# Optimization experiments

Measured on AMD Instinct MI355X. Metric: run time of the kernel, lower is better.

Reference implementation:

```python
import jax, jax.numpy as jnp
from jax import lax
import numpy as np

NBITS = 3  # PartialSumLSQ bit width


def binarize(x):
    # straight-through sign (Binarize in BNN code modifies .data -> identity STE)
    return x + lax.stop_gradient(jnp.sign(x) - x)


def lsq(y, alpha):
    # LSQ quantizer for partial sums: q = round(clamp(y/a, Qn, Qp)) * a, STE round,
    # gradient-scaled step size (forward value unaffected by g).
    Qn, Qp = -(2 ** (NBITS - 1)), 2 ** (NBITS - 1) - 1
    g = 1.0 / np.sqrt(y.size * Qp)
    a = alpha * g + lax.stop_gradient(alpha - alpha * g)
    yc = jnp.clip(y / a, Qn, Qp)
    yq = yc + lax.stop_gradient(jnp.round(yc) - yc)
    return yq * a


def split_slices(xp, cgroups):
    # xp: [B, 128*cgroups, H+2, W+2]; reproduces split_tensor_128/256/512 ordering:
    # channel group outermost, then col offset j, then row offset i.
    H, W = xp.shape[2] - 2, xp.shape[3] - 2
    sl = [xp[:, g * 128:(g + 1) * 128, i:i + H, j:j + W]
          for g in range(cgroups) for j in range(3) for i in range(3)]
    return jnp.stack(sl)  # [S, B, 128, H, W]


def psum_stage(x, w, b, alpha, cgroups):
    # emulated 3x3 binary conv: pad, split into S shifted 128-ch slices, per-slice
    # binarized 1x1 conv + bias, LSQ-quantize each partial sum, accumulate.
    xp = jnp.pad(binarize(x), ((0, 0), (0, 0), (1, 1), (1, 1)))
    xs = split_slices(xp, cgroups)                      # [S,B,128,H,W]
    y = jnp.einsum('sbchw,soc->sbohw', xs, binarize(w)) + b[:, None, :, None, None]
    return jax.vmap(lsq)(y, alpha).sum(0)               # [B,Cout,H,W]


def maxpool2(x):
    return lax.reduce_window(x, -jnp.inf, lax.max, (1, 1, 2, 2), (1, 1, 2, 2), 'VALID')


def bn(x, g, b):
    # eval-mode BatchNorm with running_mean=0, running_var=1 -> affine
    s = (1, -1) + (1,) * (x.ndim - 2)
    return x * g.reshape(s) + b.reshape(s)


def htanh(x):
    return jnp.clip(x, -1.0, 1.0)


def _forward(x, conv1_w, conv1_b, s2_w, s2_b, s2_a, s3_w, s3_b, s3_a,
             s4_w, s4_b, s4_a, s5_w, s5_b, s5_a, s6_w, s6_b, s6_a,
             bn1_g, bn1_b, bn2_g, bn2_b, bn3_g, bn3_b, bn4_g, bn4_b,
             bn5_g, bn5_b, bn6_g, bn6_b, fc1_w, fc1_b, fc2_w, fc2_b,
             fc3_w, fc3_b, fbn1_g, fbn1_b, fbn2_g, fbn2_b, fbn3_g, fbn3_b):
    # conv1: 3->128 3x3 pad1; input has 3 channels -> not binarized, weight binarized
    h = lax.conv_general_dilated(x, binarize(conv1_w), (1, 1), ((1, 1), (1, 1)),
                                 dimension_numbers=('NCHW', 'OIHW', 'NCHW'))
    h = h + conv1_b[None, :, None, None]
    h = htanh(bn(h, bn1_g, bn1_b))
    h = psum_stage(h, s2_w, s2_b, s2_a, 1)   # 128->128, 9 slices, 32x32
    h = maxpool2(h)                          # 16x16
    h = htanh(bn(h, bn2_g, bn2_b))
    h = psum_stage(h, s3_w, s3_b, s3_a, 1)   # 128->256, 9 slices
    h = htanh(bn(h, bn3_g, bn3_b))
    h = psum_stage(h, s4_w, s4_b, s4_a, 2)   # 256->256, 18 slices
    h = maxpool2(h)                          # 8x8
    h = htanh(bn(h, bn4_g, bn4_b))
    h = psum_stage(h, s5_w, s5_b, s5_a, 2)   # 256->512, 18 slices
    h = htanh(bn(h, bn5_g, bn5_b))
    h = psum_stage(h, s6_w, s6_b, s6_a, 4)   # 512->512, 36 slices
    h = maxpool2(h)                          # 4x4
    h = htanh(bn(h, bn6_g, bn6_b))
    # binarized classifier: 512*4*4 -> 1024 -> 1024 -> num_classes
    f = binarize(h.reshape(h.shape[0], -1))
    f = f @ binarize(fc1_w).T + fc1_b
    f = htanh(f * fbn1_g + fbn1_b)
    f = binarize(f) @ binarize(fc2_w).T + fc2_b
    f = htanh(f * fbn2_g + fbn2_b)
    f = binarize(f) @ binarize(fc3_w).T + fc3_b
    return f * fbn3_g + fbn3_b


def setup_inputs() -> dict:
    key = jax.random.key(0)
    ks = iter(jax.random.split(key, 80))
    def rn(shape, scale=1.0):
        return jax.random.normal(next(ks), shape, jnp.float32) * scale
    d = {}
    d['x'] = rn((64, 3, 32, 32))
    d['conv1_w'] = rn((128, 3, 3, 3), 0.1)
    d['conv1_b'] = rn((128,), 0.01)
    stages = {'s2': (9, 128), 's3': (9, 256), 's4': (18, 256),
              's5': (18, 512), 's6': (36, 512)}
    for name, (S, co) in stages.items():
        d[name + '_w'] = rn((S, co, 128), 0.1)
        d[name + '_b'] = rn((S, co), 0.01)
        d[name + '_a'] = jax.random.uniform(next(ks), (S,), jnp.float32, 0.05, 0.15)
    for i, c in zip(range(1, 7), [128, 128, 256, 256, 512, 512]):
        d[f'bn{i}_g'] = jnp.ones((c,), jnp.float32) + rn((c,), 0.01)
        d[f'bn{i}_b'] = rn((c,), 0.01)
    d['fc1_w'] = rn((1024, 512 * 16), 0.02); d['fc1_b'] = rn((1024,), 0.01)
    d['fc2_w'] = rn((1024, 1024), 0.02);     d['fc2_b'] = rn((1024,), 0.01)
    d['fc3_w'] = rn((10, 1024), 0.02);       d['fc3_b'] = rn((10,), 0.01)
    for i, c in zip(range(1, 4), [1024, 1024, 10]):
        d[f'fbn{i}_g'] = jnp.ones((c,), jnp.float32) + rn((c,), 0.01)
        d[f'fbn{i}_b'] = rn((c,), 0.01)
    return d


def reference(x, conv1_w, conv1_b, s2_w, s2_b, s2_a, s3_w, s3_b, s3_a,
              s4_w, s4_b, s4_a, s5_w, s5_b, s5_a, s6_w, s6_b, s6_a,
              bn1_g, bn1_b, bn2_g, bn2_b, bn3_g, bn3_b, bn4_g, bn4_b,
              bn5_g, bn5_b, bn6_g, bn6_b, fc1_w, fc1_b, fc2_w, fc2_b,
              fc3_w, fc3_b, fbn1_g, fbn1_b, fbn2_g, fbn2_b, fbn3_g, fbn3_b):
    return _forward(x, conv1_w, conv1_b, s2_w, s2_b, s2_a, s3_w, s3_b, s3_a,
                    s4_w, s4_b, s4_a, s5_w, s5_b, s5_a, s6_w, s6_b, s6_a,
                    bn1_g, bn1_b, bn2_g, bn2_b, bn3_g, bn3_b, bn4_g, bn4_b,
                    bn5_g, bn5_b, bn6_g, bn6_b, fc1_w, fc1_b, fc2_w, fc2_b,
                    fc3_w, fc3_b, fbn1_g, fbn1_b, fbn2_g, fbn2_b, fbn3_g, fbn3_b)
```

## Files before the change

kernel.cpp:

```cpp
#include <hip/hip_runtime.h>
#include <hip/hip_bf16.h>
#include <math.h>

typedef unsigned long long u64;

struct PrepArgs {
    const float* w[7];
    u64* out[7];
    int cnt[7];
    int mode[7];
    const float* fc1w;
    u64* fc1T;
    const float* alpha[5];
    const float* bias[5];
    int loff[5];
    int lCout[5];
    double gq[5];
    u64* wlut;
    int R1, R2, R3;
};

__global__ __launch_bounds__(256)
void k_prep(PrepArgs A) {
    int gid = blockIdx.x * 256 + threadIdx.x;
    int lane = threadIdx.x & 63;
    if (gid < A.R1) {
        int wid = gid >> 6;
        int seg = 0, base = 0, pre = 0;
#pragma unroll
        for (int t = 0; t < 7; ++t) {
            if (wid >= pre) { seg = t; base = pre; }
            pre += A.cnt[t];
        }
        int li = wid - base;
        const float* p = A.w[seg] + ((size_t)li << 6);
        u64 m = __ballot(p[lane] > 0.f);
        if (lane == 0) {
            int mode = A.mode[seg];
            size_t idx = (mode == 1) ? ((size_t)(li >> 1) * 4 + (li & 1))
                       : (mode == 2) ? ((size_t)(li & 15) * 1024 + (li >> 4))
                       : (size_t)li;
            A.out[seg][idx] = m;
        }
    } else if (gid < A.R2) {
        int wid = (gid - A.R1) >> 6;
        int row = wid >> 3, gk = wid & 7;
        int g = gk >> 1, k = gk & 1;
        int c = g * 128 + k * 64 + lane;
        const float* p = A.fc1w + (size_t)row * 8192 + (size_t)c * 16;
        float arr[16];
#pragma unroll
        for (int q = 0; q < 4; ++q) {
            float4 f = ((const float4*)p)[q];
            arr[4 * q + 0] = f.x; arr[4 * q + 1] = f.y;
            arr[4 * q + 2] = f.z; arr[4 * q + 3] = f.w;
        }
#pragma unroll
        for (int h = 0; h < 4; ++h)
#pragma unroll
        for (int xq = 0; xq < 4; ++xq) {
            u64 m = __ballot(arr[h * 4 + xq] > 0.f);
            if (lane == 0) {
                int wd = g * 32 + h * 8 + xq * 2 + k;
                A.fc1T[(size_t)wd * 1024 + row] = m;
            }
        }
    } else if (gid < A.R3) {
        int idx = gid - A.R2;
        int seg = 0;
#pragma unroll
        for (int t = 1; t < 5; ++t) if (idx >= A.loff[t]) seg = t;
        int li = idx - A.loff[seg];
        int s = li / A.lCout[seg];
        double al = (double)A.alpha[seg][s];
        double tg = al * A.gq[seg];
        double a  = tg + (al - tg);
        double b  = (double)A.bias[seg][li];
        double q0 = rint(fmin(fmax(b / a, -4.0), 3.0));
        double qp = rint(fmin(fmax((2.0 + b) / a, -4.0), 3.0));
        double qn = rint(fmin(fmax((-2.0 + b) / a, -4.0), 3.0));
        double cz = q0 * a;
        double dp = qp * a - cz, dn = qn * a - cz;
        A.wlut[(size_t)idx * 4 + 2] = __double_as_longlong(0.5 * (dp + dn));
        A.wlut[(size_t)idx * 4 + 3] = __double_as_longlong(0.5 * (dp - dn));
    }
}

struct PvArgs {
    const float* alpha[5];
    const float* bias[5];
    int rowoff[5];
    int czoff[5];
    int S[5];
    int Cout[5];
    double gq[5];
    int total;
};

__global__ void k_pv(PvArgs A, const u64* __restrict__ wlut,
                     double* __restrict__ czv, double* __restrict__ pvt) {
    int idx = blockIdx.x * blockDim.x + threadIdx.x;
    if (idx >= A.total) return;
    int seg = 0;
#pragma unroll
    for (int t = 1; t < 5; ++t) if (idx >= A.czoff[t]) seg = t;
    int o = idx - A.czoff[seg];
    int Cout = A.Cout[seg];
    double CZ = 0.0;
    double pv[8] = {0, 0, 0, 0, 0, 0, 0, 0};
    for (int s = 0; s < A.S[seg]; ++s) {
        double al = (double)A.alpha[seg][s];
        double tg = al * A.gq[seg];
        double a  = tg + (al - tg);
        double b  = (double)A.bias[seg][s * Cout + o];
        double q0 = rint(fmin(fmax(b / a, -4.0), 3.0));
        CZ += q0 * a;
        size_t so = (size_t)(A.rowoff[seg] + s * Cout + o);
        const u64* wl = wlut + so * 4;
        u64 w0 = wl[0], w1 = wl[1];
        double mid  = __longlong_as_double(wl[2]);
        double half = __longlong_as_double(wl[3]);
        int e0 = 64 - (__popcll(w0) + __popcll(w1));
        int sg = min(max(e0, -1), 1);
        double sd = (double)sg;
        double pvv = fma(sd, fma(mid, sd, half), 0.0);
        int i3 = s % 3, j3 = (s / 3) % 3;
        if (i3 == 0) { pv[0] += pvv; if (j3 == 0) pv[4] += pvv; if (j3 == 2) pv[6] += pvv; }
        if (i3 == 2) { pv[1] += pvv; if (j3 == 0) pv[5] += pvv; if (j3 == 2) pv[7] += pvv; }
        if (j3 == 0) pv[2] += pvv;
        if (j3 == 2) pv[3] += pvv;
    }
    czv[idx] = CZ;
#pragma unroll
    for (int k = 0; k < 8; ++k) pvt[(size_t)idx * 8 + k] = pv[k];
}

__global__ __launch_bounds__(128)
void k_conv1(const float* __restrict__ x, const float* __restrict__ w,
             const float* __restrict__ cb, const float* __restrict__ g1,
             const float* __restrict__ b1, u64* __restrict__ apack) {
    __shared__ double xs[3][3][34];
    int h = blockIdx.x & 31;
    int b = blockIdx.x >> 5;
    int tid = threadIdx.x;
    for (int idx = tid; idx < 306; idx += 128) {
        int dyy = idx / 102;
        int rem = idx - dyy * 102;
        int ci = rem / 34;
        int col = rem - ci * 34;
        int y = h + dyy - 1, xx = col - 1;
        double v = 0.0;
        if ((unsigned)y < 32u && (unsigned)xx < 32u)
            v = (double)x[((b * 3 + ci) * 32 + y) * 32 + xx];
        xs[dyy][ci][col] = v;
    }
    __syncthreads();
    int o = tid;
    double sg[3][3][3];
#pragma unroll
    for (int ci = 0; ci < 3; ++ci)
#pragma unroll
    for (int ky = 0; ky < 3; ++ky)
#pragma unroll
    for (int kx = 0; kx < 3; ++kx) {
        float wv = w[o * 27 + (ci * 3 + ky) * 3 + kx];
        sg[kx][ci][ky] = wv > 0.f ? 1.0 : (wv < 0.f ? -1.0 : 0.0);
    }
    double cbv = (double)cb[o], g1v = (double)g1[o], b1v = (double)b1[o];
    double A0 = 0.0, A1 = 0.0, A2 = 0.0;
    for (int pc = 0; pc < 34; ++pc) {
        double v[3][3];
#pragma unroll
        for (int ky = 0; ky < 3; ++ky)
#pragma unroll
        for (int ci = 0; ci < 3; ++ci)
            v[ky][ci] = xs[ky][ci][pc];
        A2 = 0.0;
#pragma unroll
        for (int ci = 0; ci < 3; ++ci)
#pragma unroll
        for (int ky = 0; ky < 3; ++ky) {
            A0 += v[ky][ci] * sg[2][ci][ky];
            A1 += v[ky][ci] * sg[1][ci][ky];
            A2 += v[ky][ci] * sg[0][ci][ky];
        }
        if (pc >= 2) {
            int wc = pc - 2;
            double t = (A0 + cbv) * g1v + b1v;
            u64 m = __ballot(t > 0.0);
            if ((tid & 63) == 0)
                apack[((size_t)(b * 1024 + h * 32 + wc)) * 2 + (tid >> 6)] = m;
        }
        A0 = A1; A1 = A2;
    }
}

template <int POOL, int G, int H, int W, int Cout, int RCH, int NCH>
__global__ __launch_bounds__(64 * RCH * NCH)
void k_stage(const u64* __restrict__ apack, const u64* __restrict__ wlut,
             const double* __restrict__ czv, const double* __restrict__ pvt,
             const float* __restrict__ gam, const float* __restrict__ bet,
             u64* __restrict__ opack) {
    constexpr int CW = W / NCH;
    constexpr int Ho = H / POOL, Wo = W / POOL;
    constexpr int NOC = Cout / 64;
    constexpr int NRB = H / RCH;
    constexpr int NT = 64 * RCH * NCH;
    constexpr int NR = RCH + 2;
    constexpr int NCOL = W + 2;
    __shared__ alignas(16) u64 sact[G][NR][NCOL][2];
    constexpr int PLP = (POOL == 2) ? (RCH / 2) : 1;
    constexpr int PLN = (POOL == 2) ? NCH : 1;
    constexpr int PLC = (POOL == 2) ? (CW / 2) : 1;
    __shared__ double pl[PLP][PLN][PLC][64];

    int bi = blockIdx.x;
    int och = bi % NOC; bi /= NOC;
    int rb = bi % NRB;
    int b = bi / NRB;
    int tid = threadIdx.x;
    int ol = tid & 63;
    int rr = tid >> 6;
    int rc = rr / NCH;
    int nc = rr - rc * NCH;
    int o = och * 64 + ol;
    int yr = rb * RCH + rc;
    int c0 = nc * CW;

    for (int t = tid; t < G * NR * NCOL; t += NT) {
        int g = t / (NR * NCOL);
        int r2 = t - g * (NR * NCOL);
        int yy = r2 / NCOL;
        int xx = r2 - yy * NCOL;
        int y = rb * RCH + yy - 1;
        int x = xx - 1;
        u64 v0 = 0, v1 = 0;
        if ((unsigned)y < (unsigned)H && (unsigned)x < (unsigned)W) {
            const u64* p = apack + ((size_t)((b * G + g) * H + y) * W + x) * 2;
            v0 = p[0]; v1 = p[1];
        }
        sact[g][yy][xx][0] = v0;
        sact[g][yy][xx][1] = v1;
    }
    __syncthreads();

    double CZ = czv[o];
    double acc[CW];
#pragma unroll
    for (int c = 0; c < CW; ++c) acc[c] = CZ;

#pragma unroll 1
    for (int g = 0; g < G; ++g) {
#pragma unroll
        for (int i = 0; i < 3; ++i) {
            const int yy = rc + i;
            ulonglong2 ar[CW + 2];
#pragma unroll
            for (int k = 0; k < CW + 2; ++k)
                ar[k] = *(const ulonglong2*)&sact[g][yy][c0 + k][0];
#pragma unroll
            for (int j = 0; j < 3; ++j) {
                int s = g * 9 + j * 3 + i;
                size_t so = (size_t)s * Cout + o;
                ulonglong2 wv = *(const ulonglong2*)(wlut + so * 4);
                ulonglong2 mh = *(const ulonglong2*)(wlut + so * 4 + 2);
                u64 w0 = wv.x, w1 = wv.y;
                double mid  = __longlong_as_double(mh.x);
                double half = __longlong_as_double(mh.y);
#pragma unroll
                for (int c = 0; c < CW; ++c) {
                    u64 a0 = ar[c + j].x, a1 = ar[c + j].y;
                    int d = __popcll(a0 ^ w0) + __popcll(a1 ^ w1);
                    int e = 64 - d;
                    int sg = min(max(e, -1), 1);
                    double sd = (double)sg;
                    acc[c] = fma(sd, fma(mid, sd, half), acc[c]);
                }
            }
        }
    }

    const double* pvo = pvt + (size_t)o * 8;
    if (yr == 0) {
        double v = pvo[0];
#pragma unroll
        for (int c = 0; c < CW; ++c) acc[c] -= v;
    }
    if (yr == H - 1) {
        double v = pvo[1];
#pragma unroll
        for (int c = 0; c < CW; ++c) acc[c] -= v;
    }
    if (nc == 0) {
        acc[0] -= pvo[2];
        if (yr == 0)     acc[0] += pvo[4];
        if (yr == H - 1) acc[0] += pvo[5];
    }
    if (nc == NCH - 1) {
        acc[CW - 1] -= pvo[3];
        if (yr == 0)     acc[CW - 1] += pvo[6];
        if (yr == H - 1) acc[CW - 1] += pvo[7];
    }

    double gv = (double)gam[o], bv = (double)bet[o];
    if constexpr (POOL == 1) {
#pragma unroll
        for (int c = 0; c < CW; ++c) {
            double t = acc[c] * gv + bv;
            u64 bm = __ballot(t > 0.0);
            if (ol == 0) {
                int pw = c0 + c;
                opack[(((size_t)(b * (Cout >> 7) + (o >> 7)) * Ho + yr) * Wo + pw) * 2
                      + (och & 1)] = bm;
            }
        }
    } else {
        double m2[CW / 2];
#pragma unroll
        for (int c2 = 0; c2 < CW / 2; ++c2)
            m2[c2] = fmax(acc[2 * c2], acc[2 * c2 + 1]);
        if (rc & 1) {
#pragma unroll
            for (int c2 = 0; c2 < CW / 2; ++c2)
                pl[rc >> 1][nc][c2][ol] = m2[c2];
        }
        __syncthreads();
        if (!(rc & 1)) {
#pragma unroll
            for (int c2 = 0; c2 < CW / 2; ++c2) {
                double m = fmax(m2[c2], pl[rc >> 1][nc][c2][ol]);
                double t = m * gv + bv;
                u64 bm = __ballot(t > 0.0);
                if (ol == 0) {
                    int ph = yr >> 1;
                    int pw = (c0 >> 1) + c2;
                    opack[(((size_t)(b * (Cout >> 7) + (o >> 7)) * Ho + ph) * Wo + pw) * 2
                          + (och & 1)] = bm;
                }
            }
        }
    }
}

__global__ __launch_bounds__(1024)
void k_fc_all(const u64* __restrict__ abits, const u64* __restrict__ wf1T,
              const float* __restrict__ b1, const float* __restrict__ g1,
              const float* __restrict__ a1,
              const u64* __restrict__ wf2T,
              const float* __restrict__ b2, const float* __restrict__ g2,
              const float* __restrict__ a2,
              const u64* __restrict__ wf3,
              const float* __restrict__ b3, const float* __restrict__ g3,
              const float* __restrict__ a3,
              float* __restrict__ out) {
    __shared__ u64 sa[128];
    __shared__ u64 sp1[16];
    __shared__ u64 sp2[16];
    int b = blockIdx.x;
    int t = threadIdx.x;
    if (t < 128) sa[t] = abits[(size_t)b * 128 + t];
    __syncthreads();
    {
        int d = 0;
#pragma unroll 16
        for (int i = 0; i < 128; ++i)
            d += __popcll(sa[i] ^ wf1T[(size_t)i * 1024 + t]);
        double isum = (double)(8192 - 2 * d);
        double v = (isum + (double)b1[t]) * (double)g1[t] + (double)a1[t];
        u64 m = __ballot(v > 0.0);
        if ((t & 63) == 0) sp1[t >> 6] = m;
    }
    __syncthreads();
    {
        int d = 0;
#pragma unroll
        for (int i = 0; i < 16; ++i)
            d += __popcll(sp1[i] ^ wf2T[(size_t)i * 1024 + t]);
        double isum = (double)(1024 - 2 * d);
        double v = (isum + (double)b2[t]) * (double)g2[t] + (double)a2[t];
        u64 m = __ballot(v > 0.0);
        if ((t & 63) == 0) sp2[t >> 6] = m;
    }
    __syncthreads();
    if (t < 10) {
        int d = 0;
#pragma unroll
        for (int i = 0; i < 16; ++i)
            d += __popcll(sp2[i] ^ wf3[t * 16 + i]);
        double isum = (double)(1024 - 2 * d);
        out[b * 10 + t] = (float)((isum + (double)b3[t]) * (double)g3[t] + (double)a3[t]);
    }
}


extern "C" void kernel_launch(void* const* d_in, const int* in_sizes, int n_in,
                              void* d_out, int out_size, void* d_ws, size_t ws_size,
                              hipStream_t stream) {
    const float* x       = (const float*)d_in[0];
    const float* conv1_w = (const float*)d_in[1];
    const float* conv1_b = (const float*)d_in[2];
    const float* s_w[5]  = {(const float*)d_in[3], (const float*)d_in[6], (const float*)d_in[9],
                            (const float*)d_in[12], (const float*)d_in[15]};
    const float* s_b[5]  = {(const float*)d_in[4], (const float*)d_in[7], (const float*)d_in[10],
                            (const float*)d_in[13], (const float*)d_in[16]};
    const float* s_a[5]  = {(const float*)d_in[5], (const float*)d_in[8], (const float*)d_in[11],
                            (const float*)d_in[14], (const float*)d_in[17]};
    const float* bn_g[6], *bn_b[6];
    for (int i = 0; i < 6; ++i) { bn_g[i] = (const float*)d_in[18 + 2 * i]; bn_b[i] = (const float*)d_in[19 + 2 * i]; }
    const float* fc1_w = (const float*)d_in[30]; const float* fc1_b = (const float*)d_in[31];
    const float* fc2_w = (const float*)d_in[32]; const float* fc2_b = (const float*)d_in[33];
    const float* fc3_w = (const float*)d_in[34]; const float* fc3_b = (const float*)d_in[35];
    const float* fbn_g[3], *fbn_b[3];
    for (int i = 0; i < 3; ++i) { fbn_g[i] = (const float*)d_in[36 + 2 * i]; fbn_b[i] = (const float*)d_in[37 + 2 * i]; }

    size_t off = 0;
    auto alloc = [&](size_t bytes) { off = (off + 255) & ~(size_t)255; size_t o = off; off += bytes; return o; };
    char* ws = (char*)d_ws;
    size_t o_apA  = alloc(1048576);
    size_t o_apB  = alloc(1048576);
    size_t o_wlut = alloc((size_t)35712 * 4 * 8);
    size_t o_cz   = alloc((size_t)1664 * 8);
    size_t o_pvt  = alloc((size_t)1664 * 8 * 8);
    size_t o_wf1  = alloc((size_t)1024 * 128 * 8);
    size_t o_wf2  = alloc((size_t)1024 * 16 * 8);
    size_t o_wf3  = alloc((size_t)160 * 8);
    if (off > ws_size) return;

    u64* apA = (u64*)(ws + o_apA);
    u64* apB = (u64*)(ws + o_apB);
    u64* wlut = (u64*)(ws + o_wlut);
    double* czbuf = (double*)(ws + o_cz);
    double* pvbuf = (double*)(ws + o_pvt);
    u64* wf1T = (u64*)(ws + o_wf1);
    u64* wf2T = (u64*)(ws + o_wf2);
    u64* wf3 = (u64*)(ws + o_wf3);

    const int rowoff[5] = {0, 1152, 3456, 8064, 17280};
    const int czoff[5]  = {0, 128, 384, 640, 1152};
    const int sS[5]     = {9, 9, 18, 18, 36};
    const int sCout[5]  = {128, 256, 256, 512, 512};
    const double sYsz[5] = {8388608.0, 4194304.0, 4194304.0, 2097152.0, 2097152.0};

    PrepArgs PA;
    const int scnt[5] = {2304, 4608, 9216, 18432, 36864};
    int totw = 0;
    for (int i = 0; i < 5; ++i) {
        PA.w[i] = s_w[i];
        PA.out[i] = wlut + (size_t)rowoff[i] * 4;
        PA.cnt[i] = scnt[i];
        PA.mode[i] = 1;
        totw += scnt[i];
    }
    PA.w[5] = fc2_w; PA.out[5] = wf2T; PA.cnt[5] = 1024 * 16; PA.mode[5] = 2; totw += 1024 * 16;
    PA.w[6] = fc3_w; PA.out[6] = wf3;  PA.cnt[6] = 160;       PA.mode[6] = 0; totw += 160;
    PA.fc1w = fc1_w; PA.fc1T = wf1T;
    for (int i = 0; i < 5; ++i) {
        PA.alpha[i] = s_a[i]; PA.bias[i] = s_b[i];
        PA.loff[i] = rowoff[i]; PA.lCout[i] = sCout[i];
        PA.gq[i] = 1.0 / sqrt(sYsz[i] * 3.0);
    }
    PA.wlut = wlut;
    PA.R1 = totw * 64;
    PA.R2 = PA.R1 + 1024 * 8 * 64;
    PA.R3 = PA.R2 + 35712;
    k_prep<<<(PA.R3 + 255) / 256, 256, 0, stream>>>(PA);

    PvArgs VA;
    for (int i = 0; i < 5; ++i) {
        VA.alpha[i] = s_a[i]; VA.bias[i] = s_b[i];
        VA.rowoff[i] = rowoff[i]; VA.czoff[i] = czoff[i];
        VA.S[i] = sS[i]; VA.Cout[i] = sCout[i];
        VA.gq[i] = 1.0 / sqrt(sYsz[i] * 3.0);
    }
    VA.total = 1664;
    k_pv<<<(1664 + 255) / 256, 256, 0, stream>>>(VA, wlut, czbuf, pvbuf);

    k_conv1<<<64 * 32, 128, 0, stream>>>(x, conv1_w, conv1_b, bn_g[0], bn_b[0], apA);

    k_stage<2, 1, 32, 32, 128, 2, 4><<<64 * 16 * 2, 512, 0, stream>>>(
        apA, wlut + (size_t)rowoff[0] * 4, czbuf + czoff[0], pvbuf + (size_t)czoff[0] * 8,
        bn_g[1], bn_b[1], apB);
    k_stage<1, 1, 16, 16, 256, 2, 2><<<64 * 8 * 4, 256, 0, stream>>>(
        apB, wlut + (size_t)rowoff[1] * 4, czbuf + czoff[1], pvbuf + (size_t)czoff[1] * 8,
        bn_g[2], bn_b[2], apA);
    k_stage<2, 2, 16, 16, 256, 2, 2><<<64 * 8 * 4, 256, 0, stream>>>(
        apA, wlut + (size_t)rowoff[2] * 4, czbuf + czoff[2], pvbuf + (size_t)czoff[2] * 8,
        bn_g[3], bn_b[3], apB);
    k_stage<1, 2, 8, 8, 512, 2, 1><<<64 * 4 * 8, 128, 0, stream>>>(
        apB, wlut + (size_t)rowoff[3] * 4, czbuf + czoff[3], pvbuf + (size_t)czoff[3] * 8,
        bn_g[4], bn_b[4], apA);
    k_stage<2, 4, 8, 8, 512, 2, 1><<<64 * 4 * 8, 128, 0, stream>>>(
        apA, wlut + (size_t)rowoff[4] * 4, czbuf + czoff[4], pvbuf + (size_t)czoff[4] * 8,
        bn_g[5], bn_b[5], apB);

    k_fc_all<<<64, 1024, 0, stream>>>(apB, wf1T, fc1_b, fbn_g[0], fbn_b[0],
                                      wf2T, fc2_b, fbn_g[1], fbn_b[1],
                                      wf3, fc3_b, fbn_g[2], fbn_b[2],
                                      (float*)d_out);
}
```

Baseline: 238.6 us.

## Split channel groups across wavefronts in late binary conv stages

Adds a GS template parameter that splits the channel-group loop of k_stage across two wavefronts. The partial accumulators are combined through shared memory before the edge correction and BN/binarize epilogue, and the two smallest stages (8x8, 512 channels) now launch with 256 threads. This aims to raise parallelism and latency hiding in stages that had only 128 threads per block and few blocks, at the cost of extra shared memory, a __syncthreads, and wavefronts that sit idle during the epilogue.

```diff
diff --git a/kernel.cpp b/kernel.cpp
--- a/kernel.cpp
+++ b/kernel.cpp
@@ -195,8 +195,8 @@
     }
 }
 
-template <int POOL, int G, int H, int W, int Cout, int RCH, int NCH>
-__global__ __launch_bounds__(64 * RCH * NCH)
+template <int POOL, int G, int GS, int H, int W, int Cout, int RCH, int NCH>
+__global__ __launch_bounds__(64 * RCH * NCH * GS)
 void k_stage(const u64* __restrict__ apack, const u64* __restrict__ wlut,
              const double* __restrict__ czv, const double* __restrict__ pvt,
              const float* __restrict__ gam, const float* __restrict__ bet,
@@ -205,14 +205,15 @@
     constexpr int Ho = H / POOL, Wo = W / POOL;
     constexpr int NOC = Cout / 64;
     constexpr int NRB = H / RCH;
-    constexpr int NT = 64 * RCH * NCH;
+    constexpr int NT = 64 * RCH * NCH * GS;
     constexpr int NR = RCH + 2;
     constexpr int NCOL = W + 2;
+    constexpr int GH = G / GS;
     __shared__ alignas(16) u64 sact[G][NR][NCOL][2];
-    constexpr int PLP = (POOL == 2) ? (RCH / 2) : 1;
-    constexpr int PLN = (POOL == 2) ? NCH : 1;
-    constexpr int PLC = (POOL == 2) ? (CW / 2) : 1;
-    __shared__ double pl[PLP][PLN][PLC][64];
+    constexpr int CMB = (GS == 2) ? (RCH * NCH * CW * 64) : 1;
+    __shared__ double comb[CMB];
+    constexpr int PLSZ = (POOL == 2) ? ((RCH / 2) * NCH * (CW / 2) * 64) : 1;
+    __shared__ double pl[PLSZ];
 
     int bi = blockIdx.x;
     int och = bi % NOC; bi /= NOC;
@@ -220,9 +221,10 @@
     int b = bi / NRB;
     int tid = threadIdx.x;
     int ol = tid & 63;
-    int rr = tid >> 6;
-    int rc = rr / NCH;
-    int nc = rr - rc * NCH;
+    int wv = tid >> 6;
+    int gs = wv % GS;
+    int nc = (wv / GS) % NCH;
+    int rc = wv / (GS * NCH);
     int o = och * 64 + ol;
     int yr = rb * RCH + rc;
     int c0 = nc * CW;
@@ -244,13 +246,16 @@
     }
     __syncthreads();
 
-    double CZ = czv[o];
     double acc[CW];
-#pragma unroll
-    for (int c = 0; c < CW; ++c) acc[c] = CZ;
+    {
+        double init = (GS == 1 || gs == 0) ? czv[o] : 0.0;
+#pragma unroll
+        for (int c = 0; c < CW; ++c) acc[c] = init;
+    }
 
 #pragma unroll 1
-    for (int g = 0; g < G; ++g) {
+    for (int gg = 0; gg < GH; ++gg) {
+        const int g = gs * GH + gg;
 #pragma unroll
         for (int i = 0; i < 3; ++i) {
             const int yy = rc + i;
@@ -262,9 +267,9 @@
             for (int j = 0; j < 3; ++j) {
                 int s = g * 9 + j * 3 + i;
                 size_t so = (size_t)s * Cout + o;
-                ulonglong2 wv = *(const ulonglong2*)(wlut + so * 4);
+                ulonglong2 wvv = *(const ulonglong2*)(wlut + so * 4);
                 ulonglong2 mh = *(const ulonglong2*)(wlut + so * 4 + 2);
-                u64 w0 = wv.x, w1 = wv.y;
+                u64 w0 = wvv.x, w1 = wvv.y;
                 double mid  = __longlong_as_double(mh.x);
                 double half = __longlong_as_double(mh.y);
 #pragma unroll
@@ -280,55 +285,78 @@
         }
     }
 
-    const double* pvo = pvt + (size_t)o * 8;
-    if (yr == 0) {
-        double v = pvo[0];
-#pragma unroll
-        for (int c = 0; c < CW; ++c) acc[c] -= v;
-    }
-    if (yr == H - 1) {
-        double v = pvo[1];
-#pragma unroll
-        for (int c = 0; c < CW; ++c) acc[c] -= v;
-    }
-    if (nc == 0) {
-        acc[0] -= pvo[2];
-        if (yr == 0)     acc[0] += pvo[4];
-        if (yr == H - 1) acc[0] += pvo[5];
-    }
-    if (nc == NCH - 1) {
-        acc[CW - 1] -= pvo[3];
-        if (yr == 0)     acc[CW - 1] += pvo[6];
-        if (yr == H - 1) acc[CW - 1] += pvo[7];
+    if constexpr (GS == 2) {
+        if (gs == 1) {
+#pragma unroll
+            for (int c = 0; c < CW; ++c)
+                comb[(((size_t)rc * NCH + nc) * CW + c) * 64 + ol] = acc[c];
+        }
+        __syncthreads();
+        if (gs == 0) {
+#pragma unroll
+            for (int c = 0; c < CW; ++c)
+                acc[c] += comb[(((size_t)rc * NCH + nc) * CW + c) * 64 + ol];
+        }
+    }
+
+    const bool act = (GS == 1) || (gs == 0);
+
+    if (act) {
+        const double* pvo = pvt + (size_t)o * 8;
+        if (yr == 0) {
+            double v = pvo[0];
+#pragma unroll
+            for (int c = 0; c < CW; ++c) acc[c] -= v;
+        }
+        if (yr == H - 1) {
+            double v = pvo[1];
+#pragma unroll
+            for (int c = 0; c < CW; ++c) acc[c] -= v;
+        }
+        if (nc == 0) {
+            acc[0] -= pvo[2];
+            if (yr == 0)     acc[0] += pvo[4];
+            if (yr == H - 1) acc[0] += pvo[5];
+        }
+        if (nc == NCH - 1) {
+            acc[CW - 1] -= pvo[3];
+            if (yr == 0)     acc[CW - 1] += pvo[6];
+            if (yr == H - 1) acc[CW - 1] += pvo[7];
+        }
     }
 
     double gv = (double)gam[o], bv = (double)bet[o];
     if constexpr (POOL == 1) {
-#pragma unroll
-        for (int c = 0; c < CW; ++c) {
-            double t = acc[c] * gv + bv;
-            u64 bm = __ballot(t > 0.0);
-            if (ol == 0) {
-                int pw = c0 + c;
-                opack[(((size_t)(b * (Cout >> 7) + (o >> 7)) * Ho + yr) * Wo + pw) * 2
-                      + (och & 1)] = bm;
+        if (act) {
+#pragma unroll
+            for (int c = 0; c < CW; ++c) {
+                double t = acc[c] * gv + bv;
+                u64 bm = __ballot(t > 0.0);
+                if (ol == 0) {
+                    int pw = c0 + c;
+                    opack[(((size_t)(b * (Cout >> 7) + (o >> 7)) * Ho + yr) * Wo + pw) * 2
+                          + (och & 1)] = bm;
+                }
             }
         }
     } else {
         double m2[CW / 2];
-#pragma unroll
-        for (int c2 = 0; c2 < CW / 2; ++c2)
-            m2[c2] = fmax(acc[2 * c2], acc[2 * c2 + 1]);
-        if (rc & 1) {
+        if (act) {
 #pragma unroll
             for (int c2 = 0; c2 < CW / 2; ++c2)
-                pl[rc >> 1][nc][c2][ol] = m2[c2];
+                m2[c2] = fmax(acc[2 * c2], acc[2 * c2 + 1]);
+            if (rc & 1) {
+#pragma unroll
+                for (int c2 = 0; c2 < CW / 2; ++c2)
+                    pl[((((size_t)(rc >> 1) * NCH + nc) * (CW / 2)) + c2) * 64 + ol] = m2[c2];
+            }
         }
         __syncthreads();
-        if (!(rc & 1)) {
+        if (act && !(rc & 1)) {
 #pragma unroll
             for (int c2 = 0; c2 < CW / 2; ++c2) {
-                double m = fmax(m2[c2], pl[rc >> 1][nc][c2][ol]);
+                double m = fmax(m2[c2],
+                                pl[((((size_t)(rc >> 1) * NCH + nc) * (CW / 2)) + c2) * 64 + ol]);
                 double t = m * gv + bv;
                 u64 bm = __ballot(t > 0.0);
                 if (ol == 0) {
@@ -477,19 +505,19 @@
 
     k_conv1<<<64 * 32, 128, 0, stream>>>(x, conv1_w, conv1_b, bn_g[0], bn_b[0], apA);
 
-    k_stage<2, 1, 32, 32, 128, 2, 4><<<64 * 16 * 2, 512, 0, stream>>>(
+    k_stage<2, 1, 1, 32, 32, 128, 2, 4><<<64 * 16 * 2, 512, 0, stream>>>(
         apA, wlut + (size_t)rowoff[0] * 4, czbuf + czoff[0], pvbuf + (size_t)czoff[0] * 8,
         bn_g[1], bn_b[1], apB);
-    k_stage<1, 1, 16, 16, 256, 2, 2><<<64 * 8 * 4, 256, 0, stream>>>(
+    k_stage<1, 1, 1, 16, 16, 256, 2, 2><<<64 * 8 * 4, 256, 0, stream>>>(
         apB, wlut + (size_t)rowoff[1] * 4, czbuf + czoff[1], pvbuf + (size_t)czoff[1] * 8,
         bn_g[2], bn_b[2], apA);
-    k_stage<2, 2, 16, 16, 256, 2, 2><<<64 * 8 * 4, 256, 0, stream>>>(
+    k_stage<2, 2, 1, 16, 16, 256, 2, 2><<<64 * 8 * 4, 256, 0, stream>>>(
         apA, wlut + (size_t)rowoff[2] * 4, czbuf + czoff[2], pvbuf + (size_t)czoff[2] * 8,
         bn_g[3], bn_b[3], apB);
-    k_stage<1, 2, 8, 8, 512, 2, 1><<<64 * 4 * 8, 128, 0, stream>>>(
+    k_stage<1, 2, 2, 8, 8, 512, 2, 1><<<64 * 4 * 8, 256, 0, stream>>>(
         apB, wlut + (size_t)rowoff[3] * 4, czbuf + czoff[3], pvbuf + (size_t)czoff[3] * 8,
         bn_g[4], bn_b[4], apA);
-    k_stage<2, 4, 8, 8, 512, 2, 1><<<64 * 4 * 8, 128, 0, stream>>>(
+    k_stage<2, 4, 2, 8, 8, 512, 2, 1><<<64 * 4 * 8, 256, 0, stream>>>(
         apA, wlut + (size_t)rowoff[4] * 4, czbuf + czoff[4], pvbuf + (size_t)czoff[4] * 8,
         bn_g[5], bn_b[5], apB);
 
```

Result: no change. 234.6 us (-1.7%).
